# Kernel optimization log

Hardware: AMD Instinct MI355X
Metric: run time of the kernel (lower is better)

Reference implementation:

```python
import jax, jax.numpy as jnp
import numpy as np
import math

N_QUBITS = 10
N_LAYERS = 2
HIDDEN = 768
VOCAB = 30522
DIM = 2 ** N_QUBITS


def _cnot_perm(c, t, n):
    # PennyLane convention: wire 0 is the most significant bit of the basis index.
    idx = np.arange(2 ** n)
    ctrl_bit = (idx >> (n - 1 - c)) & 1
    return jnp.asarray(idx ^ (ctrl_bit << (n - 1 - t)))

# BasicEntanglerLayers uses a CNOT ring: (0,1),(1,2),...,(n-1,0)
CNOT_PERMS = [_cnot_perm(q, (q + 1) % N_QUBITS, N_QUBITS) for q in range(N_QUBITS)]


def _apply_rx(state, theta, q):
    # state: (N, 2^n) complex, theta: (N,) per-sample RX angle on wire q.
    c = jnp.cos(theta * 0.5)[:, None, None]
    s = jnp.sin(theta * 0.5)[:, None, None]
    st = state.reshape(-1, 2 ** q, 2, DIM // (2 ** (q + 1)))
    a0, a1 = st[:, :, 0, :], st[:, :, 1, :]
    b0 = c * a0 - 1j * s * a1
    b1 = c * a1 - 1j * s * a0
    return jnp.stack([b0, b1], axis=2).reshape(state.shape)


def _quantum_probs(angles):
    # angles: (N, L, n). BasicEntanglerLayers = per-layer RX rotations + CNOT ring,
    # followed by qml.probs over all wires -> (N, 2^n).
    N = angles.shape[0]
    state = jnp.zeros((N, DIM), jnp.complex64).at[:, 0].set(1.0)
    for l in range(N_LAYERS):
        for q in range(N_QUBITS):
            state = _apply_rx(state, angles[:, l, q], q)
        for q in range(N_QUBITS):
            state = state[:, CNOT_PERMS[q]]
    return state.real ** 2 + state.imag ** 2


def _gelu(x):
    return x * 0.5 * (1.0 + jax.scipy.special.erf(x / math.sqrt(2.0)))


def setup_inputs() -> dict:
    key = jax.random.key(0)
    ks = jax.random.split(key, 4)
    B, S = 8, 512
    return {
        "hidden_states": jax.random.normal(ks[0], (B, S, HIDDEN), jnp.float32),
        "dense_w": jax.random.normal(ks[1], (HIDDEN, HIDDEN), jnp.float32) * 0.02,
        "dense_b": jnp.zeros((HIDDEN,), jnp.float32),
        "ln_w": jnp.ones((HIDDEN,), jnp.float32),
        "ln_b": jnp.zeros((HIDDEN,), jnp.float32),
        "ent_w": jax.random.normal(ks[2], (HIDDEN, N_LAYERS * N_QUBITS), jnp.float32) * 0.02,
        "ent_b": jnp.zeros((N_LAYERS * N_QUBITS,), jnp.float32),
        "proj_w": jax.random.normal(ks[3], (DIM, VOCAB), jnp.float32) * 0.02,
        "proj_b": jnp.zeros((VOCAB,), jnp.float32),
    }


def reference(hidden_states, dense_w, dense_b, ln_w, ln_b, ent_w, ent_b, proj_w, proj_b):
    # BertPredictionHeadTransform: dense -> gelu -> LayerNorm (eps inside sqrt)
    h = _gelu(hidden_states @ dense_w + dense_b)
    u = h.mean(-1, keepdims=True)
    v = ((h - u) ** 2).mean(-1, keepdims=True)
    h = ln_w * ((h - u) / jnp.sqrt(v + 1e-12)) + ln_b
    # entangle params -> sigmoid * 2pi, flatten batch to (N, L, n)
    ang = jax.nn.sigmoid(h @ ent_w + ent_b).reshape(-1, N_LAYERS, N_QUBITS) * (2.0 * math.pi)
    probs = _quantum_probs(ang)  # (B*S, 2^n)
    return probs @ proj_w + proj_b  # (B*S, vocab)
```

## Files before the change

kernel.cpp:

```cpp
#include <hip/hip_runtime.h>
#include <hip/hip_bf16.h>
#include <math.h>

#define HIDDEN 768
#define NROWS 4096
#define QDIM 1024
#define VOCAB 30522
#define NPAD 30592

typedef _Float16 half8 __attribute__((ext_vector_type(8)));
typedef float floatx4 __attribute__((ext_vector_type(4)));

__global__ __launch_bounds__(1024) void convert_transpose(
    const float* __restrict__ B, _Float16* __restrict__ BT) {
  __shared__ _Float16 tile[32][33];
  int n0 = blockIdx.x * 32;
  int k0 = blockIdx.y * 32;
  int tx = threadIdx.x, ty = threadIdx.y;
  int n = n0 + tx, k = k0 + ty;
  float v = (n < VOCAB) ? B[k * VOCAB + n] : 0.0f;
  tile[ty][tx] = (_Float16)v;
  __syncthreads();
  BT[(n0 + ty) * QDIM + (k0 + tx)] = tile[tx][ty];
}

__global__ __launch_bounds__(256) void gemm1_gelu(
    const float* __restrict__ A, const float* __restrict__ W,
    const float* __restrict__ bias, float* __restrict__ H) {
  __shared__ float As[64][17];
  __shared__ float Bs[16][68];
  int t = threadIdx.x;
  int bm = blockIdx.y * 64, bn = blockIdx.x * 64;
  int tx = t & 15, ty = t >> 4;
  float acc[4][4] = {};
  for (int k0 = 0; k0 < HIDDEN; k0 += 16) {
    {
      int r = t >> 2, c = (t & 3) * 4;
      float4 v = *(const float4*)&A[(bm + r) * HIDDEN + k0 + c];
      As[r][c] = v.x; As[r][c + 1] = v.y; As[r][c + 2] = v.z; As[r][c + 3] = v.w;
    }
    {
      int kr = t >> 4, c = (t & 15) * 4;
      float4 v = *(const float4*)&W[(k0 + kr) * HIDDEN + bn + c];
      Bs[kr][c] = v.x; Bs[kr][c + 1] = v.y; Bs[kr][c + 2] = v.z; Bs[kr][c + 3] = v.w;
    }
    __syncthreads();
#pragma unroll
    for (int k = 0; k < 16; k++) {
      float a[4], b[4];
#pragma unroll
      for (int i = 0; i < 4; i++) a[i] = As[ty * 4 + i][k];
#pragma unroll
      for (int j = 0; j < 4; j++) b[j] = Bs[k][tx * 4 + j];
#pragma unroll
      for (int i = 0; i < 4; i++)
#pragma unroll
        for (int j = 0; j < 4; j++) acc[i][j] += a[i] * b[j];
    }
    __syncthreads();
  }
#pragma unroll
  for (int i = 0; i < 4; i++) {
    int m = bm + ty * 4 + i;
#pragma unroll
    for (int j = 0; j < 4; j++) {
      int n = bn + tx * 4 + j;
      float x = acc[i][j] + bias[n];
      float g = x * 0.5f * (1.0f + erff(x * 0.70710678118654752f));
      H[m * HIDDEN + n] = g;
    }
  }
}

__device__ inline float block_sum256(float v, float* red) {
  int t = threadIdx.x;
#pragma unroll
  for (int o = 32; o > 0; o >>= 1) v += __shfl_down(v, o);
  __syncthreads();
  if ((t & 63) == 0) red[t >> 6] = v;
  __syncthreads();
  return red[0] + red[1] + red[2] + red[3];
}

__global__ __launch_bounds__(256) void row_quantum(
    const float* __restrict__ H, const float* __restrict__ ln_w,
    const float* __restrict__ ln_b, const float* __restrict__ ent_w,
    const float* __restrict__ ent_b, _Float16* __restrict__ probsA) {
  __shared__ float hn[HIDDEN];
  __shared__ float red[4];
  __shared__ float sr[QDIM];
  __shared__ float si[QDIM];
  __shared__ float ang[20];
  int t = threadIdx.x;
  int row = blockIdx.x;
  const float* hr = H + row * HIDDEN;

  float sum = 0.f;
  for (int i = t; i < HIDDEN; i += 256) {
    float v = hr[i];
    hn[i] = v;
    sum += v;
  }
  float u = block_sum256(sum, red) * (1.0f / HIDDEN);
  float vs = 0.f;
  for (int i = t; i < HIDDEN; i += 256) {
    float d = hn[i] - u;
    vs += d * d;
  }
  float var = block_sum256(vs, red) * (1.0f / HIDDEN);
  float inv = rsqrtf(var + 1e-12f);
  for (int i = t; i < HIDDEN; i += 256)
    hn[i] = ln_w[i] * ((hn[i] - u) * inv) + ln_b[i];
  __syncthreads();

  if (t < 20) {
    float acc = ent_b[t];
#pragma unroll 4
    for (int i = 0; i < HIDDEN; i++) acc += hn[i] * ent_w[i * 20 + t];
    float s = 1.0f / (1.0f + expf(-acc));
    ang[t] = 6.283185307179586f * s;
  }
  __syncthreads();

  for (int i = t; i < QDIM; i += 256) {
    sr[i] = (i == 0) ? 1.0f : 0.0f;
    si[i] = 0.0f;
  }
  __syncthreads();

  for (int l = 0; l < 2; l++) {
    for (int q = 0; q < 10; q++) {
      float th = ang[l * 10 + q] * 0.5f;
      float c, s;
      __sincosf(th, &s, &c);
      s = sinf(th); c = cosf(th);
      int bp = 9 - q;
      int mask = 1 << bp;
#pragma unroll
      for (int p = 0; p < 2; p++) {
        int pi = t + p * 256;
        int i0 = ((pi >> bp) << (bp + 1)) | (pi & (mask - 1));
        int i1 = i0 | mask;
        float a0r = sr[i0], a0i = si[i0], a1r = sr[i1], a1i = si[i1];
        sr[i0] = c * a0r + s * a1i;
        si[i0] = c * a0i - s * a1r;
        sr[i1] = c * a1r + s * a0i;
        si[i1] = c * a1i - s * a0r;
      }
      __syncthreads();
    }
    float tr[4], ti[4];
#pragma unroll
    for (int p = 0; p < 4; p++) {
      int i = t + p * 256;
      int j = i;
#pragma unroll
      for (int q = 9; q >= 0; q--) {
        int cb = 9 - q;
        int tb = 9 - ((q + 1) % 10);
        j ^= ((j >> cb) & 1) << tb;
      }
      tr[p] = sr[j];
      ti[p] = si[j];
    }
    __syncthreads();
#pragma unroll
    for (int p = 0; p < 4; p++) {
      int i = t + p * 256;
      sr[i] = tr[p];
      si[i] = ti[p];
    }
    __syncthreads();
  }

  for (int i = t; i < QDIM; i += 256) {
    float pv = sr[i] * sr[i] + si[i] * si[i];
    probsA[row * QDIM + i] = (_Float16)pv;
  }
}

__global__ __launch_bounds__(256) void gemm2_mfma(
    const _Float16* __restrict__ A,
    const _Float16* __restrict__ BT,
    const float* __restrict__ bias,
    float* __restrict__ C) {
  __shared__ _Float16 As[128][40];
  __shared__ _Float16 Bs[128][40];
  int t = threadIdx.x;
  int lane = t & 63, wave = t >> 6;
  int quad = lane >> 4, ln = lane & 15;
  int wm = (wave >> 1) * 64, wn = (wave & 1) * 64;
  int bm = blockIdx.y * 128;
  int bn = blockIdx.x * 128;

  floatx4 acc[4][4];
#pragma unroll
  for (int i = 0; i < 4; i++)
#pragma unroll
    for (int j = 0; j < 4; j++) acc[i][j] = (floatx4){0.f, 0.f, 0.f, 0.f};

  for (int k0 = 0; k0 < QDIM; k0 += 32) {
    __syncthreads();
#pragma unroll
    for (int cch = 0; cch < 2; cch++) {
      int idx = t + cch * 256;
      int r = idx >> 2, col = (idx & 3) * 8;
      *(half8*)&As[r][col] = *(const half8*)&A[(bm + r) * QDIM + k0 + col];
      *(half8*)&Bs[r][col] = *(const half8*)&BT[(bn + r) * QDIM + k0 + col];
    }
    __syncthreads();
    half8 a[4], b[4];
#pragma unroll
    for (int i = 0; i < 4; i++) a[i] = *(const half8*)&As[wm + i * 16 + ln][quad * 8];
#pragma unroll
    for (int j = 0; j < 4; j++) b[j] = *(const half8*)&Bs[wn + j * 16 + ln][quad * 8];
#pragma unroll
    for (int i = 0; i < 4; i++)
#pragma unroll
      for (int j = 0; j < 4; j++)
        acc[i][j] = __builtin_amdgcn_mfma_f32_16x16x32_f16(a[i], b[j], acc[i][j], 0, 0, 0);
  }

#pragma unroll
  for (int j = 0; j < 4; j++) {
    int n = bn + wn + j * 16 + ln;
    if (n >= VOCAB) continue;
    float bv = bias[n];
#pragma unroll
    for (int i = 0; i < 4; i++) {
#pragma unroll
      for (int r = 0; r < 4; r++) {
        int m = bm + wm + i * 16 + quad * 4 + r;
        C[(size_t)m * VOCAB + n] = acc[i][j][r] + bv;
      }
    }
  }
}

extern "C" void kernel_launch(void* const* d_in, const int* in_sizes, int n_in,
                              void* d_out, int out_size, void* d_ws, size_t ws_size,
                              hipStream_t stream) {
  const float* hs      = (const float*)d_in[0];
  const float* dense_w = (const float*)d_in[1];
  const float* dense_b = (const float*)d_in[2];
  const float* ln_w    = (const float*)d_in[3];
  const float* ln_b    = (const float*)d_in[4];
  const float* ent_w   = (const float*)d_in[5];
  const float* ent_b   = (const float*)d_in[6];
  const float* proj_w  = (const float*)d_in[7];
  const float* proj_b  = (const float*)d_in[8];
  float* out = (float*)d_out;

  char* ws = (char*)d_ws;
  float*     h      = (float*)ws;
  _Float16*  probsA = (_Float16*)(ws + 12582912);
  _Float16*  BT     = (_Float16*)(ws + 20971520);

  hipLaunchKernelGGL(convert_transpose, dim3(NPAD / 32, QDIM / 32), dim3(32, 32), 0, stream,
                     proj_w, BT);
  hipLaunchKernelGGL(gemm1_gelu, dim3(HIDDEN / 64, NROWS / 64), dim3(256), 0, stream,
                     hs, dense_w, dense_b, h);
  hipLaunchKernelGGL(row_quantum, dim3(NROWS), dim3(256), 0, stream,
                     h, ln_w, ln_b, ent_w, ent_b, probsA);
  hipLaunchKernelGGL(gemm2_mfma, dim3(NPAD / 128, NROWS / 128), dim3(256), 0, stream,
                     probsA, BT, proj_b, out);
}
```

Baseline: 1.229 ms.

## Use direct global-to-LDS loads with XOR swizzle and tile remap in output GEMM

The output GEMM now loads A and B tiles straight into shared memory with global_load_lds, using an XOR-swizzled layout in place of padding to avoid bank conflicts. The K step grows from 32 to 64, which halves the number of barrier pairs per tile. The grid becomes one-dimensional and workgroup IDs are remapped into eight groups to improve L2 locality across blocks. The redundant duplicate sin/cos computation in the quantum kernel is also dropped. There is still no double buffering, so loads do not overlap with compute.

Measured after the change: 1.274 ms. 1.04x slower.

```diff
diff --git a/kernel.cpp b/kernel.cpp
--- a/kernel.cpp
+++ b/kernel.cpp
@@ -7,9 +7,18 @@
 #define QDIM 1024
 #define VOCAB 30522
 #define NPAD 30592
+#define NBX 239
+#define NBY 32
+#define NWG (NBX * NBY)
 
 typedef _Float16 half8 __attribute__((ext_vector_type(8)));
 typedef float floatx4 __attribute__((ext_vector_type(4)));
+
+__device__ __forceinline__ void gload16(const _Float16* g, _Float16* l) {
+  __builtin_amdgcn_global_load_lds(
+      (const __attribute__((address_space(1))) void*)g,
+      (__attribute__((address_space(3))) void*)l, 16, 0, 0);
+}
 
 __global__ __launch_bounds__(1024) void convert_transpose(
     const float* __restrict__ B, _Float16* __restrict__ BT) {
@@ -131,9 +140,7 @@
   for (int l = 0; l < 2; l++) {
     for (int q = 0; q < 10; q++) {
       float th = ang[l * 10 + q] * 0.5f;
-      float c, s;
-      __sincosf(th, &s, &c);
-      s = sinf(th); c = cosf(th);
+      float c = cosf(th), s = sinf(th);
       int bp = 9 - q;
       int mask = 1 << bp;
 #pragma unroll
@@ -184,14 +191,30 @@
     const _Float16* __restrict__ BT,
     const float* __restrict__ bias,
     float* __restrict__ C) {
-  __shared__ _Float16 As[128][40];
-  __shared__ _Float16 Bs[128][40];
+  __shared__ _Float16 As[128][64];
+  __shared__ _Float16 Bs[128][64];
+
   int t = threadIdx.x;
   int lane = t & 63, wave = t >> 6;
   int quad = lane >> 4, ln = lane & 15;
   int wm = (wave >> 1) * 64, wn = (wave & 1) * 64;
-  int bm = blockIdx.y * 128;
-  int bn = blockIdx.x * 128;
+
+  int wg = blockIdx.x;
+  int swz = (wg & 7) * (NWG / 8) + (wg >> 3);
+  int bn = (swz >> 5) * 128;
+  int bm = (swz & 31) * 128;
+
+  int srow = t >> 3;
+  int ps = t & 7;
+  int lslot = ps ^ (srow & 7);
+  const _Float16* gA = A  + (size_t)(bm + srow) * QDIM + lslot * 8;
+  const _Float16* gB = BT + (size_t)(bn + srow) * QDIM + lslot * 8;
+  _Float16* lA = &As[srow][ps * 8];
+  _Float16* lB = &Bs[srow][ps * 8];
+
+  int r7 = ln & 7;
+  int off0 = ((0 * 4 + quad) ^ r7) * 8;
+  int off1 = ((1 * 4 + quad) ^ r7) * 8;
 
   floatx4 acc[4][4];
 #pragma unroll
@@ -199,26 +222,28 @@
 #pragma unroll
     for (int j = 0; j < 4; j++) acc[i][j] = (floatx4){0.f, 0.f, 0.f, 0.f};
 
-  for (int k0 = 0; k0 < QDIM; k0 += 32) {
-    __syncthreads();
-#pragma unroll
-    for (int cch = 0; cch < 2; cch++) {
-      int idx = t + cch * 256;
-      int r = idx >> 2, col = (idx & 3) * 8;
-      *(half8*)&As[r][col] = *(const half8*)&A[(bm + r) * QDIM + k0 + col];
-      *(half8*)&Bs[r][col] = *(const half8*)&BT[(bn + r) * QDIM + k0 + col];
-    }
-    __syncthreads();
-    half8 a[4], b[4];
-#pragma unroll
-    for (int i = 0; i < 4; i++) a[i] = *(const half8*)&As[wm + i * 16 + ln][quad * 8];
-#pragma unroll
-    for (int j = 0; j < 4; j++) b[j] = *(const half8*)&Bs[wn + j * 16 + ln][quad * 8];
-#pragma unroll
-    for (int i = 0; i < 4; i++)
-#pragma unroll
-      for (int j = 0; j < 4; j++)
-        acc[i][j] = __builtin_amdgcn_mfma_f32_16x16x32_f16(a[i], b[j], acc[i][j], 0, 0, 0);
+  for (int k0 = 0; k0 < QDIM; k0 += 64) {
+#pragma unroll
+    for (int i = 0; i < 4; i++) {
+      gload16(gA + (size_t)i * 32 * QDIM + k0, lA + i * 32 * 64);
+      gload16(gB + (size_t)i * 32 * QDIM + k0, lB + i * 32 * 64);
+    }
+    __syncthreads();
+#pragma unroll
+    for (int s = 0; s < 2; s++) {
+      int off = s ? off1 : off0;
+      half8 a[4], b[4];
+#pragma unroll
+      for (int i = 0; i < 4; i++) a[i] = *(const half8*)&As[wm + i * 16 + ln][off];
+#pragma unroll
+      for (int j = 0; j < 4; j++) b[j] = *(const half8*)&Bs[wn + j * 16 + ln][off];
+#pragma unroll
+      for (int i = 0; i < 4; i++)
+#pragma unroll
+        for (int j = 0; j < 4; j++)
+          acc[i][j] = __builtin_amdgcn_mfma_f32_16x16x32_f16(a[i], b[j], acc[i][j], 0, 0, 0);
+    }
+    __syncthreads();
   }
 
 #pragma unroll
@@ -262,6 +287,6 @@
                      hs, dense_w, dense_b, h);
   hipLaunchKernelGGL(row_quantum, dim3(NROWS), dim3(256), 0, stream,
                      h, ln_w, ln_b, ent_w, ent_b, probsA);
-  hipLaunchKernelGGL(gemm2_mfma, dim3(NPAD / 128, NROWS / 128), dim3(256), 0, stream,
+  hipLaunchKernelGGL(gemm2_mfma, dim3(NWG), dim3(256), 0, stream,
                      probsA, BT, proj_b, out);
 }
```
